# Optimization experiments

Measured on AMD Instinct MI355X. Metric: run time of the kernel, lower is better.

The kernel has to match this reference:

```python
import jax, jax.numpy as jnp
import numpy as np

B, N = 16, 16384
K = 16        # num_keypoints
LATENT = 128
CAGE = 8
BN_EPS = 1e-5


def setup_inputs():
    key = jax.random.key(0)
    ks = jax.random.split(key, 40)
    def rn(i, shape, s=1.0):
        return jax.random.normal(ks[i], shape, dtype=jnp.float32) * s
    inp = {
        "source_points": rn(0, (B, N, 3)),
        "target_points": rn(1, (B, N, 3)),
        "enc_w1": rn(2, (64, 3), 0.3), "enc_b1": rn(3, (64,), 0.1),
        "bn1_gamma": 1.0 + rn(4, (64,), 0.1), "bn1_beta": rn(5, (64,), 0.1),
        "bn1_mean": rn(6, (64,), 0.1), "bn1_var": 0.5 + jax.random.uniform(ks[7], (64,), dtype=jnp.float32),
        "enc_w2": rn(8, (128, 64), 0.1), "enc_b2": rn(9, (128,), 0.1),
        "bn2_gamma": 1.0 + rn(10, (128,), 0.1), "bn2_beta": rn(11, (128,), 0.1),
        "bn2_mean": rn(12, (128,), 0.1), "bn2_var": 0.5 + jax.random.uniform(ks[13], (128,), dtype=jnp.float32),
        "enc_w3": rn(14, (LATENT, 128), 0.1), "enc_b3": rn(15, (LATENT,), 0.1),
        "bn3_gamma": 1.0 + rn(16, (LATENT,), 0.1), "bn3_beta": rn(17, (LATENT,), 0.1),
        "bn3_mean": rn(18, (LATENT,), 0.1), "bn3_var": 0.5 + jax.random.uniform(ks[19], (LATENT,), dtype=jnp.float32),
        "kp_w1": rn(20, (128, LATENT), 0.1), "kp_b1": rn(21, (128,), 0.1),
        "kp_w2": rn(22, (K * 3, 128), 0.1), "kp_b2": rn(23, (K * 3,), 0.1),
        "cg_w1": rn(24, (128, K * 3), 0.1), "cg_b1": rn(25, (128,), 0.1),
        "cg_w2": rn(26, (CAGE ** 3 * 3, 128), 0.05), "cg_b2": rn(27, (CAGE ** 3 * 3,), 0.01),
    }
    return inp


def _bn(x, g, b, m, v):
    # inference-mode BatchNorm1d over channel (last) dim
    return (x - m) * jax.lax.rsqrt(v + BN_EPS) * g + b


def _encode(pts, w1, b1, g1, be1, m1, v1, w2, b2, g2, be2, m2, v2, w3, b3, g3, be3, m3, v3):
    # pointwise 1x1 convs == per-point linear layers; pts: (B, N, 3)
    h = jax.nn.relu(_bn(jnp.einsum('bnc,oc->bno', pts, w1) + b1, g1, be1, m1, v1))
    h = jax.nn.relu(_bn(jnp.einsum('bnc,oc->bno', h, w2) + b2, g2, be2, m2, v2))
    h = jax.nn.relu(_bn(jnp.einsum('bnc,oc->bno', h, w3) + b3, g3, be3, m3, v3))
    return h.max(axis=1)  # global max-pool -> (B, LATENT)


def _fps_one(pts, kps):
    # pts: (N,3), kps: (K,3). Same math as the torch loop: iterative farthest-point
    # selection; recomputing cdist to selected[:i] each step == incremental min-dist.
    # squared distances preserve argmax/min of euclidean distances.
    d0 = jnp.sum((pts[:, None, :] - kps[None, :, :]) ** 2, -1).min(axis=1)
    sel0 = pts[jnp.argmax(d0)]
    mind = jnp.sum((pts - sel0) ** 2, -1)
    def step(mind, _):
        sel = pts[jnp.argmax(mind)]
        return jnp.minimum(mind, jnp.sum((pts - sel) ** 2, -1)), sel
    _, sels = jax.lax.scan(step, mind, None, length=K - 1)
    return jnp.concatenate([sel0[None], sels], axis=0)  # (K, 3)


def _fps(points, keypoints):
    return jax.vmap(_fps_one)(points, keypoints)


def _cage_deform(pts, disp):
    # pts: (B,N,3), disp: (B,C,C,C,3). Batched trilinear interpolation on the cage.
    C = CAGE
    lin = jnp.linspace(0.0, 1.0, C)
    grid = jnp.stack(jnp.meshgrid(lin, lin, lin, indexing='ij'), axis=-1)
    cage = grid[None] + disp
    cf = cage.reshape(cage.shape[0], C * C * C, 3)
    pmin = pts.min(axis=1, keepdims=True)
    pmax = pts.max(axis=1, keepdims=True)
    t = (pts - pmin) / (pmax - pmin + 1e-6) * (C - 1)
    idx = jnp.clip(t.astype(jnp.int32), 0, C - 2)   # trunc == floor (t >= 0)
    w = t - idx.astype(t.dtype)
    u, v, z = idx[..., 0], idx[..., 1], idx[..., 2]
    wx, wy, wz = w[..., 0:1], w[..., 1:2], w[..., 2:3]
    def corner(du, dv, dz):
        flat = (u + du) * C * C + (v + dv) * C + (z + dz)      # (B,N)
        flat = jnp.broadcast_to(flat[..., None], flat.shape + (3,))
        return jnp.take_along_axis(cf, flat, axis=1)            # (B,N,3)
    d = ((1 - wx) * (1 - wy) * (1 - wz) * corner(0, 0, 0)
         + wx * (1 - wy) * (1 - wz) * corner(1, 0, 0)
         + (1 - wx) * wy * (1 - wz) * corner(0, 1, 0)
         + wx * wy * (1 - wz) * corner(1, 1, 0)
         + (1 - wx) * (1 - wy) * wz * corner(0, 0, 1)
         + wx * (1 - wy) * wz * corner(1, 0, 1)
         + (1 - wx) * wy * wz * corner(0, 1, 1)
         + wx * wy * wz * corner(1, 1, 1))
    return pts + d


def reference(source_points, target_points, enc_w1, enc_b1, bn1_gamma, bn1_beta, bn1_mean, bn1_var, enc_w2, enc_b2, bn2_gamma, bn2_beta, bn2_mean, bn2_var, enc_w3, enc_b3, bn3_gamma, bn3_beta, bn3_mean, bn3_var, kp_w1, kp_b1, kp_w2, kp_b2, cg_w1, cg_b1, cg_w2, cg_b2):
    enc = lambda p: _encode(p, enc_w1, enc_b1, bn1_gamma, bn1_beta, bn1_mean, bn1_var,
                            enc_w2, enc_b2, bn2_gamma, bn2_beta, bn2_mean, bn2_var,
                            enc_w3, enc_b3, bn3_gamma, bn3_beta, bn3_mean, bn3_var)
    src_lat = enc(source_points)
    tgt_lat = enc(target_points)
    kp = lambda lat: (jax.nn.relu(lat @ kp_w1.T + kp_b1) @ kp_w2.T + kp_b2).reshape(-1, K, 3)
    src_kp = _fps(source_points, kp(src_lat))
    tgt_kp = _fps(target_points, kp(tgt_lat))
    diff = (tgt_kp - src_kp).reshape(-1, K * 3)
    disp = (jax.nn.relu(diff @ cg_w1.T + cg_b1) @ cg_w2.T + cg_b2).reshape(-1, CAGE, CAGE, CAGE, 3)
    deformed = _cage_deform(source_points, disp)
    return (deformed, src_kp, tgt_kp)
```

## Files before the change

kernel.cpp:

```cpp
#include <hip/hip_runtime.h>

#define B_ 16
#define N_ 16384
#define K_ 16

enum : int {
  WS_LAT  = 0,
  WS_SEL  = 5632,
  WS_PMIN = 7168,
  WS_PMAX = 7216,
  WS_CF   = 7264,
  WS_W1F  = 31840,
  WS_B1F  = 32032,
  WS_WB2H = 32096,
  WS_WB2L = 36192,
  WS_B2F  = 40288,
  WS_WB3H = 40416,
  WS_B3F  = 56800,
  WS_WB3L = 56928,
  WS_END  = 73312
};

enum : int { OUT_DEF=0, OUT_SRCKP=786432, OUT_TGTKP=787200 };

typedef _Float16 f16x8 __attribute__((ext_vector_type(8)));
typedef _Float16 f16x2 __attribute__((ext_vector_type(2)));
typedef float    f32x4 __attribute__((ext_vector_type(4)));

__device__ __forceinline__ float dist2rn(float px,float py,float pz,float sx,float sy,float sz){
  float dx=__fsub_rn(px,sx), dy=__fsub_rn(py,sy), dz=__fsub_rn(pz,sz);
  return __fadd_rn(__fadd_rn(__fmul_rn(dx,dx),__fmul_rn(dy,dy)),__fmul_rn(dz,dz));
}

__device__ __forceinline__ unsigned enc_ord(float x){
  unsigned u = __float_as_uint(x);
  return (u & 0x80000000u) ? ~u : (u | 0x80000000u);
}
__device__ __forceinline__ float dec_ord(unsigned e){
  return __uint_as_float((e & 0x80000000u) ? (e & 0x7fffffffu) : ~e);
}

struct EncW {
  const float *w1,*b1,*g1,*be1,*m1,*v1;
  const float *w2,*b2,*g2,*be2,*m2,*v2;
  const float *w3,*b3,*g3,*be3,*m3,*v3;
};

__device__ __forceinline__ float bn_scale(const float* g, const float* v, int ch){
  return g[ch] * (1.0f / sqrtf(v[ch] + 1e-5f));
}

__global__ void prep_kernel(EncW a, float* ws){
  const int stride = gridDim.x*blockDim.x;
  const int tid = blockIdx.x*blockDim.x + threadIdx.x;
  for (int i=tid;i<4096;i+=stride)
    ws[WS_LAT+i] = 0.0f;
  for (int i=tid;i<48;i+=stride){
    ((unsigned*)ws)[WS_PMIN+i] = 0xFFFFFFFFu;
    ((unsigned*)ws)[WS_PMAX+i] = 0u;
  }
  for (int i=tid;i<192;i+=stride){
    int o=i/3;
    ws[WS_W1F+i] = a.w1[i] * bn_scale(a.g1,a.v1,o);
  }
  for (int i=tid;i<64;i+=stride){
    float s = bn_scale(a.g1,a.v1,i);
    ws[WS_B1F+i] = (a.b1[i] - a.m1[i])*s + a.be1[i];
  }
  for (int i=tid;i<8192;i+=stride){
    int j = i & 7, frag = i >> 3;
    int l = frag & 63, nk = frag >> 6;
    int kt = nk & 1, nt = nk >> 1;
    int c = kt*32 + ((l>>4)<<3) + j;
    int o = nt*16 + (l&15);
    float v = a.w2[o*64+c] * bn_scale(a.g2,a.v2,o);
    _Float16 h = (_Float16)v;
    ((_Float16*)(ws+WS_WB2H))[i] = h;
    ((_Float16*)(ws+WS_WB2L))[i] = (_Float16)(v - (float)h);
  }
  for (int i=tid;i<128;i+=stride){
    float s = bn_scale(a.g2,a.v2,i);
    ws[WS_B2F+i] = (a.b2[i] - a.m2[i])*s + a.be2[i];
  }
  for (int i=tid;i<32768;i+=stride){
    int j = i & 7, frag = i >> 3;
    int l = frag & 63, nk = frag >> 6;
    int kt = nk & 3, nt = nk >> 2;
    int c = kt*32 + ((l>>4)<<3) + j;
    int o = nt*16 + (l&15);
    float v = a.w3[o*128+c] * bn_scale(a.g3,a.v3,o);
    _Float16 h = (_Float16)v;
    ((_Float16*)(ws+WS_WB3H))[i] = h;
    ((_Float16*)(ws+WS_WB3L))[i] = (_Float16)(v - (float)h);
  }
  for (int i=tid;i<128;i+=stride){
    float s = bn_scale(a.g3,a.v3,i);
    ws[WS_B3F+i] = (a.b3[i] - a.m3[i])*s + a.be3[i];
  }
}

__global__ __launch_bounds__(256) void minmax_kernel(const float* __restrict__ src,
                                                     float* __restrict__ ws){
  const int b = blockIdx.y, c = blockIdx.x, t = threadIdx.x;
  const float4* b4 = (const float4*)(src + (size_t)b*N_*3 + (size_t)c*2048*3 + (size_t)t*24);
  float a[24];
  #pragma unroll
  for (int q=0;q<6;q++){ float4 v=b4[q]; a[q*4]=v.x; a[q*4+1]=v.y; a[q*4+2]=v.z; a[q*4+3]=v.w; }
  float mn[3]={3.4e38f,3.4e38f,3.4e38f}, mx[3]={-3.4e38f,-3.4e38f,-3.4e38f};
  #pragma unroll
  for (int k=0;k<8;k++){
    mn[0]=fminf(mn[0],a[k*3  ]); mx[0]=fmaxf(mx[0],a[k*3  ]);
    mn[1]=fminf(mn[1],a[k*3+1]); mx[1]=fmaxf(mx[1],a[k*3+1]);
    mn[2]=fminf(mn[2],a[k*3+2]); mx[2]=fmaxf(mx[2],a[k*3+2]);
  }
  #pragma unroll
  for (int m=1;m<64;m<<=1){
    #pragma unroll
    for (int cc=0;cc<3;cc++){
      mn[cc]=fminf(mn[cc],__shfl_xor(mn[cc],m,64));
      mx[cc]=fmaxf(mx[cc],__shfl_xor(mx[cc],m,64));
    }
  }
  if ((t&63)==0){
    unsigned* wsu = (unsigned*)ws;
    #pragma unroll
    for (int cc=0;cc<3;cc++){
      atomicMin(&wsu[WS_PMIN + b*3 + cc], enc_ord(mn[cc]));
      atomicMax(&wsu[WS_PMAX + b*3 + cc], enc_ord(mx[cc]));
    }
  }
}

__global__ __launch_bounds__(256, 4) void encode_kernel(const float* __restrict__ src,
                                                        const float* __restrict__ tgt,
                                                        const float* __restrict__ ws,
                                                        float* __restrict__ lat){
  const int cloud = blockIdx.y;
  const int tile  = blockIdx.x;
  const int t = threadIdx.x;
  const int lane = t & 63;
  const int wn = __builtin_amdgcn_readfirstlane(t >> 6);
  const int lr = lane & 15;
  const int lg = lane >> 4;

  __shared__ alignas(16) _Float16 A[16384];
  _Float16* AH1 = A;
  _Float16* AL1 = A + 4096;
  _Float16* AH2 = A;
  _Float16* AL2 = A + 8192;

  const float* base = ((cloud < B_) ? (src + (size_t)cloud*N_*3)
                                    : (tgt + (size_t)(cloud-B_)*N_*3))
                      + (size_t)tile*64*3;

  {
    const int pt = t >> 2, q = t & 3;
    const float x = base[pt*3+0], y = base[pt*3+1], z = base[pt*3+2];
    const float* w1 = ws + WS_W1F;
    const float* b1 = ws + WS_B1F;
    const int swz = (pt & 7) << 3;
    #pragma unroll
    for (int cc = 0; cc < 16; cc += 2){
      const int o = q*16 + cc;
      float v0 = fmaf(w1[o*3+2], z, fmaf(w1[o*3+1], y, w1[o*3+0]*x)) + b1[o];
      float v1 = fmaf(w1[o*3+5], z, fmaf(w1[o*3+4], y, w1[o*3+3]*x)) + b1[o+1];
      v0 = fmaxf(v0, 0.0f); v1 = fmaxf(v1, 0.0f);
      f16x2 h, l;
      h[0] = (_Float16)v0;              h[1] = (_Float16)v1;
      l[0] = (_Float16)(v0 - (float)h[0]); l[1] = (_Float16)(v1 - (float)h[1]);
      const int idx = (pt*64 + o) ^ swz;
      *(f16x2*)&AH1[idx] = h;
      *(f16x2*)&AL1[idx] = l;
    }
  }
  __syncthreads();

  f32x4 acc2[4][2];
  #pragma unroll
  for (int m=0;m<4;m++){
    #pragma unroll
    for (int n=0;n<2;n++) acc2[m][n] = (f32x4){0.f,0.f,0.f,0.f};
  }
  {
    const _Float16* wb2h = (const _Float16*)(ws + WS_WB2H);
    const _Float16* wb2l = (const _Float16*)(ws + WS_WB2L);
    const int swz = (lr & 7) << 3;
    #pragma unroll
    for (int kt=0; kt<2; kt++){
      f16x8 bh[2], bl[2];
      #pragma unroll
      for (int n=0;n<2;n++){
        const int fi = (((wn*2+n)*2 + kt)*64 + lane)*8;
        bh[n] = *(const f16x8*)(wb2h + fi);
        bl[n] = *(const f16x8*)(wb2l + fi);
      }
      #pragma unroll
      for (int m=0;m<4;m++){
        const int row = m*16 + lr;
        const int idx = (row*64 + kt*32 + lg*8) ^ swz;
        const f16x8 ah = *(const f16x8*)&AH1[idx];
        const f16x8 al = *(const f16x8*)&AL1[idx];
        #pragma unroll
        for (int n=0;n<2;n++){
          acc2[m][n] = __builtin_amdgcn_mfma_f32_16x16x32_f16(ah, bh[n], acc2[m][n], 0,0,0);
          acc2[m][n] = __builtin_amdgcn_mfma_f32_16x16x32_f16(ah, bl[n], acc2[m][n], 0,0,0);
          acc2[m][n] = __builtin_amdgcn_mfma_f32_16x16x32_f16(al, bh[n], acc2[m][n], 0,0,0);
        }
      }
    }
  }
  __syncthreads();

  {
    const float* b2 = ws + WS_B2F;
    #pragma unroll
    for (int n=0;n<2;n++){
      const int ch = wn*32 + n*16 + lr;
      const float b = b2[ch];
      #pragma unroll
      for (int m=0;m<4;m++){
        #pragma unroll
        for (int r=0;r<4;r++){
          const int row = m*16 + lg*4 + r;
          const float v = fmaxf(acc2[m][n][r] + b, 0.0f);
          const _Float16 hi = (_Float16)v;
          const _Float16 lo = (_Float16)(v - (float)hi);
          const int idx = (row*128 + ch) ^ ((row & 7) << 3);
          AH2[idx] = hi;
          AL2[idx] = lo;
        }
      }
    }
  }
  __syncthreads();

  f32x4 acc3[4][2];
  #pragma unroll
  for (int m=0;m<4;m++){
    #pragma unroll
    for (int n=0;n<2;n++) acc3[m][n] = (f32x4){0.f,0.f,0.f,0.f};
  }
  {
    const _Float16* wb3h = (const _Float16*)(ws + WS_WB3H);
    const _Float16* wb3l = (const _Float16*)(ws + WS_WB3L);
    const int swz = (lr & 7) << 3;
    #pragma unroll
    for (int kt=0; kt<4; kt++){
      f16x8 bh[2], bl[2];
      #pragma unroll
      for (int n=0;n<2;n++){
        const int fi = (((wn*2+n)*4 + kt)*64 + lane)*8;
        bh[n] = *(const f16x8*)(wb3h + fi);
        bl[n] = *(const f16x8*)(wb3l + fi);
      }
      #pragma unroll
      for (int m=0;m<4;m++){
        const int row = m*16 + lr;
        const int idx = (row*128 + kt*32 + lg*8) ^ swz;
        const f16x8 ah = *(const f16x8*)&AH2[idx];
        const f16x8 al = *(const f16x8*)&AL2[idx];
        #pragma unroll
        for (int n=0;n<2;n++){
          acc3[m][n] = __builtin_amdgcn_mfma_f32_16x16x32_f16(ah, bh[n], acc3[m][n], 0,0,0);
          acc3[m][n] = __builtin_amdgcn_mfma_f32_16x16x32_f16(ah, bl[n], acc3[m][n], 0,0,0);
          acc3[m][n] = __builtin_amdgcn_mfma_f32_16x16x32_f16(al, bh[n], acc3[m][n], 0,0,0);
        }
      }
    }
  }

  {
    const float* b3 = ws + WS_B3F;
    #pragma unroll
    for (int n=0;n<2;n++){
      const int ch = wn*32 + n*16 + lr;
      const float b = b3[ch];
      float x = 0.0f;
      #pragma unroll
      for (int m=0;m<4;m++){
        #pragma unroll
        for (int r=0;r<4;r++)
          x = fmaxf(x, acc3[m][n][r] + b);
      }
      x = fmaxf(x, __shfl_xor(x, 16, 64));
      x = fmaxf(x, __shfl_xor(x, 32, 64));
      if (lane < 16)
        atomicMax((unsigned*)(lat + cloud*128 + ch), __float_as_uint(x));
    }
  }
}

__device__ __forceinline__ void fps_round(int r, int t, int wv,
                                          float bv, int bi, float bx, float by, float bz,
                                          float (*cv)[16], int (*ci)[16],
                                          float (*cx)[16], float (*cy)[16], float (*cz)[16],
                                          float* ws, float* out, int cloud,
                                          float& s0, float& s1, float& s2){
  float v = bv; int i = bi;
  #pragma unroll
  for (int m=1;m<64;m<<=1){
    float v2=__shfl_xor(v,m,64); int i2=__shfl_xor(i,m,64);
    if (v2 > v || (v2 == v && i2 < i)){ v=v2; i=i2; }
  }
  const int p = r & 1;
  if ((i >> 4) == t){ cv[p][wv]=v; ci[p][wv]=i; cx[p][wv]=bx; cy[p][wv]=by; cz[p][wv]=bz; }
  __syncthreads();
  float wvv = cv[p][0]; int wi = ci[p][0]; int ws_slot = 0;
  #pragma unroll
  for (int e=1;e<16;e++){
    float v2=cv[p][e]; int i2=ci[p][e];
    if (v2 > wvv || (v2 == wvv && i2 < wi)){ wvv=v2; wi=i2; ws_slot=e; }
  }
  s0 = cx[p][ws_slot]; s1 = cy[p][ws_slot]; s2 = cz[p][ws_slot];
  if (t == 0){
    float* sw = ws + WS_SEL + cloud*48 + r*3;
    sw[0]=s0; sw[1]=s1; sw[2]=s2;
    size_t o = (cloud<B_) ? (size_t)(OUT_SRCKP + cloud*48 + r*3)
                          : (size_t)(OUT_TGTKP + (cloud-B_)*48 + r*3);
    out[o]=s0; out[o+1]=s1; out[o+2]=s2;
  }
}

__global__ __launch_bounds__(1024) void fps_kernel(const float* __restrict__ src,
                                                   const float* __restrict__ tgt,
                                                   const float* __restrict__ kw1,
                                                   const float* __restrict__ kb1,
                                                   const float* __restrict__ kw2,
                                                   const float* __restrict__ kb2,
                                                   float* ws, float* out){
  const int cloud = blockIdx.x; const int t = threadIdx.x;
  const int wv = t >> 6;
  const float* base = (cloud < B_) ? (src + (size_t)cloud*N_*3)
                                   : (tgt + (size_t)(cloud-B_)*N_*3);
  __shared__ float kpl[48];
  __shared__ float h[128];
  __shared__ float cv[2][16]; __shared__ int ci[2][16];
  __shared__ float cx[2][16]; __shared__ float cy[2][16]; __shared__ float cz[2][16];

  float px[16], py[16], pz[16];
  {
    const float4* b4 = (const float4*)(base + (size_t)t*48);
    float a[48];
    #pragma unroll
    for (int q=0;q<12;q++){ float4 v=b4[q]; a[q*4]=v.x; a[q*4+1]=v.y; a[q*4+2]=v.z; a[q*4+3]=v.w; }
    #pragma unroll
    for (int k=0;k<16;k++){ px[k]=a[k*3]; py[k]=a[k*3+1]; pz[k]=a[k*3+2]; }
  }

  const float* lat = ws + WS_LAT + cloud*128;
  if (t < 128){
    float acc = kb1[t];
    const float* w = kw1 + t*128;
    for (int c=0;c<128;c++) acc = fmaf(lat[c], w[c], acc);
    h[t] = fmaxf(acc, 0.0f);
  }
  __syncthreads();
  if (t < 48){
    float acc = kb2[t];
    const float* w = kw2 + t*128;
    for (int c=0;c<128;c++) acc = fmaf(h[c], w[c], acc);
    kpl[t] = acc;
  }
  __syncthreads();

  float mind[16];
  #pragma unroll
  for (int k=0;k<16;k++) mind[k] = 3.4028235e38f;
  for (int j=0;j<K_;j++){
    const float sx=kpl[j*3], sy=kpl[j*3+1], sz=kpl[j*3+2];
    #pragma unroll
    for (int k=0;k<16;k++)
      mind[k] = fminf(mind[k], dist2rn(px[k],py[k],pz[k], sx,sy,sz));
  }

  float bv = -1.0f; int bi = 0; float bx=0.f, by=0.f, bz=0.f;
  #pragma unroll
  for (int k=0;k<16;k++){
    if (mind[k] > bv){ bv=mind[k]; bi=t*16+k; bx=px[k]; by=py[k]; bz=pz[k]; }
  }
  float s0, s1, s2;
  fps_round(0, t, wv, bv, bi, bx, by, bz, cv, ci, cx, cy, cz, ws, out, cloud, s0, s1, s2);

  bv = -1.0f; bi = 0;
  #pragma unroll
  for (int k=0;k<16;k++){
    float d = dist2rn(px[k],py[k],pz[k], s0,s1,s2);
    mind[k] = d;
    if (d > bv){ bv=d; bi=t*16+k; bx=px[k]; by=py[k]; bz=pz[k]; }
  }
  fps_round(1, t, wv, bv, bi, bx, by, bz, cv, ci, cx, cy, cz, ws, out, cloud, s0, s1, s2);

  for (int r=2; r<K_; ++r){
    bv = -1.0f; bi = 0;
    #pragma unroll
    for (int k=0;k<16;k++){
      float d = dist2rn(px[k],py[k],pz[k], s0,s1,s2);
      float m = fminf(mind[k], d);
      mind[k] = m;
      if (m > bv){ bv=m; bi=t*16+k; bx=px[k]; by=py[k]; bz=pz[k]; }
    }
    fps_round(r, t, wv, bv, bi, bx, by, bz, cv, ci, cx, cy, cz, ws, out, cloud, s0, s1, s2);
  }
}

__global__ void cage_mlp_kernel(const float* __restrict__ ws,
                                const float* __restrict__ cw1, const float* __restrict__ cb1,
                                const float* __restrict__ cw2, const float* __restrict__ cb2,
                                float* __restrict__ wsm){
  const int b = blockIdx.x >> 2, part = blockIdx.x & 3;
  const int t = threadIdx.x;
  __shared__ float diff[48]; __shared__ float h[128];
  if (t<48) diff[t] = __fsub_rn(ws[WS_SEL + (B_+b)*48 + t], ws[WS_SEL + b*48 + t]);
  __syncthreads();
  if (t<128){
    const float* w = cw1 + t*48;
    float acc = cb1[t];
    for (int j=0;j<48;j++) acc = fmaf(diff[j], w[j], acc);
    h[t] = fmaxf(acc, 0.0f);
  }
  __syncthreads();
  for (int o = part*384 + t; o < part*384 + 384; o += 256){
    const float* w = cw2 + o*128;
    float acc = cb2[o];
    for (int c=0;c<128;c++) acc = fmaf(h[c], w[c], acc);
    int flat = o/3, coord = o - flat*3;
    int u = flat>>6, v=(flat>>3)&7, z=flat&7;
    int g = (coord==0)?u:((coord==1)?v:z);
    float gv = (g==7)?1.0f:(float)g*(1.0f/7.0f);
    wsm[WS_CF + b*1536 + o] = gv + acc;
  }
}

__global__ __launch_bounds__(256) void deform_kernel(const float* __restrict__ src,
                                                     const float* __restrict__ ws,
                                                     float* __restrict__ out){
  const int b = blockIdx.y;
  const int n = blockIdx.x*256 + threadIdx.x;
  __shared__ float cf[1536];
  for (int i=threadIdx.x;i<1536;i+=256) cf[i] = ws[WS_CF + b*1536 + i];
  __syncthreads();

  const float* p = src + ((size_t)b*N_ + n)*3;
  float pt[3]; int id[3]; float w[3];
  #pragma unroll
  for (int c=0;c<3;c++){
    float pv = p[c];
    float mn  = dec_ord(((const unsigned*)ws)[WS_PMIN+b*3+c]);
    float mxv = dec_ord(((const unsigned*)ws)[WS_PMAX+b*3+c]);
    float denom = __fadd_rn(__fsub_rn(mxv, mn), 1e-6f);
    float tc = __fmul_rn(__fdiv_rn(__fsub_rn(pv, mn), denom), 7.0f);
    int ic = (int)tc; ic = min(max(ic,0),6);
    pt[c]=pv; id[c]=ic; w[c]=__fsub_rn(tc, (float)ic);
  }
  const int flat = (id[0]<<6) + (id[1]<<3) + id[2];
  const float* c000 = cf + flat*3;
  const float wx=w[0], wy=w[1], wz=w[2];
  const float ux=__fsub_rn(1.0f,wx), uy=__fsub_rn(1.0f,wy), uz=__fsub_rn(1.0f,wz);
  const float w000=__fmul_rn(__fmul_rn(ux,uy),uz);
  const float w100=__fmul_rn(__fmul_rn(wx,uy),uz);
  const float w010=__fmul_rn(__fmul_rn(ux,wy),uz);
  const float w110=__fmul_rn(__fmul_rn(wx,wy),uz);
  const float w001=__fmul_rn(__fmul_rn(ux,uy),wz);
  const float w101=__fmul_rn(__fmul_rn(wx,uy),wz);
  const float w011=__fmul_rn(__fmul_rn(ux,wy),wz);
  const float w111=__fmul_rn(__fmul_rn(wx,wy),wz);
  #pragma unroll
  for (int c=0;c<3;c++){
    float d = __fmul_rn(w000, c000[c]);
    d = __fadd_rn(d, __fmul_rn(w100, c000[192+c]));
    d = __fadd_rn(d, __fmul_rn(w010, c000[24+c]));
    d = __fadd_rn(d, __fmul_rn(w110, c000[216+c]));
    d = __fadd_rn(d, __fmul_rn(w001, c000[3+c]));
    d = __fadd_rn(d, __fmul_rn(w101, c000[195+c]));
    d = __fadd_rn(d, __fmul_rn(w011, c000[27+c]));
    d = __fadd_rn(d, __fmul_rn(w111, c000[219+c]));
    out[((size_t)b*N_+n)*3 + c] = __fadd_rn(pt[c], d);
  }
}

extern "C" void kernel_launch(void* const* d_in, const int* in_sizes, int n_in,
                              void* d_out, int out_size, void* d_ws, size_t ws_size,
                              hipStream_t stream){
  const float* src = (const float*)d_in[0];
  const float* tgt = (const float*)d_in[1];
  float* ws = (float*)d_ws;
  float* out = (float*)d_out;

  EncW ew;
  ew.w1 =(const float*)d_in[2];  ew.b1 =(const float*)d_in[3];
  ew.g1 =(const float*)d_in[4];  ew.be1=(const float*)d_in[5];
  ew.m1 =(const float*)d_in[6];  ew.v1 =(const float*)d_in[7];
  ew.w2 =(const float*)d_in[8];  ew.b2 =(const float*)d_in[9];
  ew.g2 =(const float*)d_in[10]; ew.be2=(const float*)d_in[11];
  ew.m2 =(const float*)d_in[12]; ew.v2 =(const float*)d_in[13];
  ew.w3 =(const float*)d_in[14]; ew.b3 =(const float*)d_in[15];
  ew.g3 =(const float*)d_in[16]; ew.be3=(const float*)d_in[17];
  ew.m3 =(const float*)d_in[18]; ew.v3 =(const float*)d_in[19];

  prep_kernel<<<128, 256, 0, stream>>>(ew, ws);
  minmax_kernel<<<dim3(8,16), 256, 0, stream>>>(src, ws);
  encode_kernel<<<dim3(256,32), 256, 0, stream>>>(src, tgt, ws, ws + WS_LAT);
  fps_kernel<<<32, 1024, 0, stream>>>(src, tgt,
      (const float*)d_in[20], (const float*)d_in[21],
      (const float*)d_in[22], (const float*)d_in[23], ws, out);
  cage_mlp_kernel<<<64, 256, 0, stream>>>(ws,
      (const float*)d_in[24], (const float*)d_in[25],
      (const float*)d_in[26], (const float*)d_in[27], ws);
  deform_kernel<<<dim3(64,16), 256, 0, stream>>>(src, ws, out);
}
```

Before: 319.3 us.

## Fuse minmax, FPS, cage MLP and deform into one per-batch tail kernel

Measured after the change: 449.0 us. 40.6% more time.

```diff
diff --git a/kernel.cpp b/kernel.cpp
--- a/kernel.cpp
+++ b/kernel.cpp
@@ -6,10 +6,6 @@
 
 enum : int {
   WS_LAT  = 0,
-  WS_SEL  = 5632,
-  WS_PMIN = 7168,
-  WS_PMAX = 7216,
-  WS_CF   = 7264,
   WS_W1F  = 31840,
   WS_B1F  = 32032,
   WS_WB2H = 32096,
@@ -32,14 +28,6 @@
   return __fadd_rn(__fadd_rn(__fmul_rn(dx,dx),__fmul_rn(dy,dy)),__fmul_rn(dz,dz));
 }
 
-__device__ __forceinline__ unsigned enc_ord(float x){
-  unsigned u = __float_as_uint(x);
-  return (u & 0x80000000u) ? ~u : (u | 0x80000000u);
-}
-__device__ __forceinline__ float dec_ord(unsigned e){
-  return __uint_as_float((e & 0x80000000u) ? (e & 0x7fffffffu) : ~e);
-}
-
 struct EncW {
   const float *w1,*b1,*g1,*be1,*m1,*v1;
   const float *w2,*b2,*g2,*be2,*m2,*v2;
@@ -55,10 +43,6 @@
   const int tid = blockIdx.x*blockDim.x + threadIdx.x;
   for (int i=tid;i<4096;i+=stride)
     ws[WS_LAT+i] = 0.0f;
-  for (int i=tid;i<48;i+=stride){
-    ((unsigned*)ws)[WS_PMIN+i] = 0xFFFFFFFFu;
-    ((unsigned*)ws)[WS_PMAX+i] = 0u;
-  }
   for (int i=tid;i<192;i+=stride){
     int o=i/3;
     ws[WS_W1F+i] = a.w1[i] * bn_scale(a.g1,a.v1,o);
@@ -96,38 +80,6 @@
   for (int i=tid;i<128;i+=stride){
     float s = bn_scale(a.g3,a.v3,i);
     ws[WS_B3F+i] = (a.b3[i] - a.m3[i])*s + a.be3[i];
-  }
-}
-
-__global__ __launch_bounds__(256) void minmax_kernel(const float* __restrict__ src,
-                                                     float* __restrict__ ws){
-  const int b = blockIdx.y, c = blockIdx.x, t = threadIdx.x;
-  const float4* b4 = (const float4*)(src + (size_t)b*N_*3 + (size_t)c*2048*3 + (size_t)t*24);
-  float a[24];
-  #pragma unroll
-  for (int q=0;q<6;q++){ float4 v=b4[q]; a[q*4]=v.x; a[q*4+1]=v.y; a[q*4+2]=v.z; a[q*4+3]=v.w; }
-  float mn[3]={3.4e38f,3.4e38f,3.4e38f}, mx[3]={-3.4e38f,-3.4e38f,-3.4e38f};
-  #pragma unroll
-  for (int k=0;k<8;k++){
-    mn[0]=fminf(mn[0],a[k*3  ]); mx[0]=fmaxf(mx[0],a[k*3  ]);
-    mn[1]=fminf(mn[1],a[k*3+1]); mx[1]=fmaxf(mx[1],a[k*3+1]);
-    mn[2]=fminf(mn[2],a[k*3+2]); mx[2]=fmaxf(mx[2],a[k*3+2]);
-  }
-  #pragma unroll
-  for (int m=1;m<64;m<<=1){
-    #pragma unroll
-    for (int cc=0;cc<3;cc++){
-      mn[cc]=fminf(mn[cc],__shfl_xor(mn[cc],m,64));
-      mx[cc]=fmaxf(mx[cc],__shfl_xor(mx[cc],m,64));
-    }
-  }
-  if ((t&63)==0){
-    unsigned* wsu = (unsigned*)ws;
-    #pragma unroll
-    for (int cc=0;cc<3;cc++){
-      atomicMin(&wsu[WS_PMIN + b*3 + cc], enc_ord(mn[cc]));
-      atomicMax(&wsu[WS_PMAX + b*3 + cc], enc_ord(mx[cc]));
-    }
   }
 }
 
@@ -290,12 +242,12 @@
   }
 }
 
-__device__ __forceinline__ void fps_round(int r, int t, int wv,
-                                          float bv, int bi, float bx, float by, float bz,
-                                          float (*cv)[16], int (*ci)[16],
-                                          float (*cx)[16], float (*cy)[16], float (*cz)[16],
-                                          float* ws, float* out, int cloud,
-                                          float& s0, float& s1, float& s2){
+__device__ __forceinline__ void fps_round_t(int r, int t, int wv,
+                                            float bv, int bi, float bx, float by, float bz,
+                                            float (*cv)[16], int (*ci)[16],
+                                            float (*cx)[16], float (*cy)[16], float (*cz)[16],
+                                            float* sel_buf, float* out, size_t out_base,
+                                            float& s0, float& s1, float& s2){
   float v = bv; int i = bi;
   #pragma unroll
   for (int m=1;m<64;m<<=1){
@@ -305,112 +257,153 @@
   const int p = r & 1;
   if ((i >> 4) == t){ cv[p][wv]=v; ci[p][wv]=i; cx[p][wv]=bx; cy[p][wv]=by; cz[p][wv]=bz; }
   __syncthreads();
-  float wvv = cv[p][0]; int wi = ci[p][0]; int ws_slot = 0;
+  float wvv = cv[p][0]; int wi = ci[p][0]; int slot = 0;
   #pragma unroll
   for (int e=1;e<16;e++){
     float v2=cv[p][e]; int i2=ci[p][e];
-    if (v2 > wvv || (v2 == wvv && i2 < wi)){ wvv=v2; wi=i2; ws_slot=e; }
-  }
-  s0 = cx[p][ws_slot]; s1 = cy[p][ws_slot]; s2 = cz[p][ws_slot];
+    if (v2 > wvv || (v2 == wvv && i2 < wi)){ wvv=v2; wi=i2; slot=e; }
+  }
+  s0 = cx[p][slot]; s1 = cy[p][slot]; s2 = cz[p][slot];
   if (t == 0){
-    float* sw = ws + WS_SEL + cloud*48 + r*3;
-    sw[0]=s0; sw[1]=s1; sw[2]=s2;
-    size_t o = (cloud<B_) ? (size_t)(OUT_SRCKP + cloud*48 + r*3)
-                          : (size_t)(OUT_TGTKP + (cloud-B_)*48 + r*3);
-    out[o]=s0; out[o+1]=s1; out[o+2]=s2;
-  }
-}
-
-__global__ __launch_bounds__(1024) void fps_kernel(const float* __restrict__ src,
-                                                   const float* __restrict__ tgt,
-                                                   const float* __restrict__ kw1,
-                                                   const float* __restrict__ kb1,
-                                                   const float* __restrict__ kw2,
-                                                   const float* __restrict__ kb2,
-                                                   float* ws, float* out){
-  const int cloud = blockIdx.x; const int t = threadIdx.x;
+    sel_buf[r*3]=s0; sel_buf[r*3+1]=s1; sel_buf[r*3+2]=s2;
+    out[out_base + r*3]=s0; out[out_base + r*3+1]=s1; out[out_base + r*3+2]=s2;
+  }
+}
+
+__global__ __launch_bounds__(1024) void tail_kernel(const float* __restrict__ src,
+                                                    const float* __restrict__ tgt,
+                                                    const float* __restrict__ kw1,
+                                                    const float* __restrict__ kb1,
+                                                    const float* __restrict__ kw2,
+                                                    const float* __restrict__ kb2,
+                                                    const float* __restrict__ cw1,
+                                                    const float* __restrict__ cb1,
+                                                    const float* __restrict__ cw2,
+                                                    const float* __restrict__ cb2,
+                                                    const float* __restrict__ ws,
+                                                    float* __restrict__ out){
+  const int b = blockIdx.x;
+  const int t = threadIdx.x;
   const int wv = t >> 6;
-  const float* base = (cloud < B_) ? (src + (size_t)cloud*N_*3)
-                                   : (tgt + (size_t)(cloud-B_)*N_*3);
+  const int lane = t & 63;
+
   __shared__ float kpl[48];
   __shared__ float h[128];
   __shared__ float cv[2][16]; __shared__ int ci[2][16];
   __shared__ float cx[2][16]; __shared__ float cy[2][16]; __shared__ float cz[2][16];
-
-  float px[16], py[16], pz[16];
-  {
-    const float4* b4 = (const float4*)(base + (size_t)t*48);
-    float a[48];
-    #pragma unroll
-    for (int q=0;q<12;q++){ float4 v=b4[q]; a[q*4]=v.x; a[q*4+1]=v.y; a[q*4+2]=v.z; a[q*4+3]=v.w; }
-    #pragma unroll
-    for (int k=0;k<16;k++){ px[k]=a[k*3]; py[k]=a[k*3+1]; pz[k]=a[k*3+2]; }
-  }
-
-  const float* lat = ws + WS_LAT + cloud*128;
-  if (t < 128){
-    float acc = kb1[t];
-    const float* w = kw1 + t*128;
-    for (int c=0;c<128;c++) acc = fmaf(lat[c], w[c], acc);
-    h[t] = fmaxf(acc, 0.0f);
-  }
-  __syncthreads();
-  if (t < 48){
-    float acc = kb2[t];
-    const float* w = kw2 + t*128;
-    for (int c=0;c<128;c++) acc = fmaf(h[c], w[c], acc);
-    kpl[t] = acc;
-  }
-  __syncthreads();
-
-  float mind[16];
-  #pragma unroll
-  for (int k=0;k<16;k++) mind[k] = 3.4028235e38f;
-  for (int j=0;j<K_;j++){
-    const float sx=kpl[j*3], sy=kpl[j*3+1], sz=kpl[j*3+2];
-    #pragma unroll
-    for (int k=0;k<16;k++)
-      mind[k] = fminf(mind[k], dist2rn(px[k],py[k],pz[k], sx,sy,sz));
-  }
-
-  float bv = -1.0f; int bi = 0; float bx=0.f, by=0.f, bz=0.f;
-  #pragma unroll
-  for (int k=0;k<16;k++){
-    if (mind[k] > bv){ bv=mind[k]; bi=t*16+k; bx=px[k]; by=py[k]; bz=pz[k]; }
-  }
-  float s0, s1, s2;
-  fps_round(0, t, wv, bv, bi, bx, by, bz, cv, ci, cx, cy, cz, ws, out, cloud, s0, s1, s2);
-
-  bv = -1.0f; bi = 0;
-  #pragma unroll
-  for (int k=0;k<16;k++){
-    float d = dist2rn(px[k],py[k],pz[k], s0,s1,s2);
-    mind[k] = d;
-    if (d > bv){ bv=d; bi=t*16+k; bx=px[k]; by=py[k]; bz=pz[k]; }
-  }
-  fps_round(1, t, wv, bv, bi, bx, by, bz, cv, ci, cx, cy, cz, ws, out, cloud, s0, s1, s2);
-
-  for (int r=2; r<K_; ++r){
+  __shared__ float sel_src[48]; __shared__ float sel_tgt[48];
+  __shared__ float red[96];
+  __shared__ float pmn[3]; __shared__ float pmx[3];
+  __shared__ float cf[1536];
+
+  for (int half=0; half<2; ++half){
+    const int cloud = b + half*B_;
+    const float* base = (half==0) ? (src + (size_t)b*N_*3) : (tgt + (size_t)b*N_*3);
+
+    float px[16], py[16], pz[16];
+    float mn0=3.4e38f,mn1=3.4e38f,mn2=3.4e38f, mx0=-3.4e38f,mx1=-3.4e38f,mx2=-3.4e38f;
+    {
+      const float4* b4 = (const float4*)(base + (size_t)t*48);
+      #pragma unroll
+      for (int q=0;q<4;q++){
+        float4 va=b4[q*3], vb=b4[q*3+1], vc=b4[q*3+2];
+        px[q*4  ]=va.x; py[q*4  ]=va.y; pz[q*4  ]=va.z;
+        px[q*4+1]=va.w; py[q*4+1]=vb.x; pz[q*4+1]=vb.y;
+        px[q*4+2]=vb.z; py[q*4+2]=vb.w; pz[q*4+2]=vc.x;
+        px[q*4+3]=vc.y; py[q*4+3]=vc.z; pz[q*4+3]=vc.w;
+      }
+    }
+
+    if (half==0){
+      #pragma unroll
+      for (int k=0;k<16;k++){
+        mn0=fminf(mn0,px[k]); mn1=fminf(mn1,py[k]); mn2=fminf(mn2,pz[k]);
+        mx0=fmaxf(mx0,px[k]); mx1=fmaxf(mx1,py[k]); mx2=fmaxf(mx2,pz[k]);
+      }
+      #pragma unroll
+      for (int m=1;m<64;m<<=1){
+        mn0=fminf(mn0,__shfl_xor(mn0,m,64)); mx0=fmaxf(mx0,__shfl_xor(mx0,m,64));
+        mn1=fminf(mn1,__shfl_xor(mn1,m,64)); mx1=fmaxf(mx1,__shfl_xor(mx1,m,64));
+        mn2=fminf(mn2,__shfl_xor(mn2,m,64)); mx2=fmaxf(mx2,__shfl_xor(mx2,m,64));
+      }
+      if (lane==0){
+        red[wv*6+0]=mn0; red[wv*6+1]=mn1; red[wv*6+2]=mn2;
+        red[wv*6+3]=mx0; red[wv*6+4]=mx1; red[wv*6+5]=mx2;
+      }
+      __syncthreads();
+      if (t==0){
+        float a0=red[0],a1=red[1],a2=red[2],a3=red[3],a4=red[4],a5=red[5];
+        for (int e=1;e<16;e++){
+          a0=fminf(a0,red[e*6+0]); a1=fminf(a1,red[e*6+1]); a2=fminf(a2,red[e*6+2]);
+          a3=fmaxf(a3,red[e*6+3]); a4=fmaxf(a4,red[e*6+4]); a5=fmaxf(a5,red[e*6+5]);
+        }
+        pmn[0]=a0; pmn[1]=a1; pmn[2]=a2; pmx[0]=a3; pmx[1]=a4; pmx[2]=a5;
+      }
+    }
+
+    const float* lat = ws + WS_LAT + cloud*128;
+    __syncthreads();
+    if (t < 128){
+      float acc = kb1[t];
+      const float* w = kw1 + t*128;
+      for (int c=0;c<128;c++) acc = fmaf(lat[c], w[c], acc);
+      h[t] = fmaxf(acc, 0.0f);
+    }
+    __syncthreads();
+    if (t < 48){
+      float acc = kb2[t];
+      const float* w = kw2 + t*128;
+      for (int c=0;c<128;c++) acc = fmaf(h[c], w[c], acc);
+      kpl[t] = acc;
+    }
+    __syncthreads();
+
+    float mind[16];
+    #pragma unroll
+    for (int k=0;k<16;k++) mind[k] = 3.4028235e38f;
+    for (int j=0;j<K_;j++){
+      const float sx=kpl[j*3], sy=kpl[j*3+1], sz=kpl[j*3+2];
+      #pragma unroll
+      for (int k=0;k<16;k++)
+        mind[k] = fminf(mind[k], dist2rn(px[k],py[k],pz[k], sx,sy,sz));
+    }
+
+    float* sel_buf = (half==0) ? sel_src : sel_tgt;
+    const size_t out_base = (half==0) ? (size_t)(OUT_SRCKP + b*48) : (size_t)(OUT_TGTKP + b*48);
+
+    float bv = -1.0f; int bi = 0; float bx=0.f, by=0.f, bz=0.f;
+    #pragma unroll
+    for (int k=0;k<16;k++){
+      if (mind[k] > bv){ bv=mind[k]; bi=t*16+k; bx=px[k]; by=py[k]; bz=pz[k]; }
+    }
+    float s0, s1, s2;
+    fps_round_t(0, t, wv, bv, bi, bx, by, bz, cv, ci, cx, cy, cz, sel_buf, out, out_base, s0, s1, s2);
+
     bv = -1.0f; bi = 0;
     #pragma unroll
     for (int k=0;k<16;k++){
       float d = dist2rn(px[k],py[k],pz[k], s0,s1,s2);
-      float m = fminf(mind[k], d);
-      mind[k] = m;
-      if (m > bv){ bv=m; bi=t*16+k; bx=px[k]; by=py[k]; bz=pz[k]; }
-    }
-    fps_round(r, t, wv, bv, bi, bx, by, bz, cv, ci, cx, cy, cz, ws, out, cloud, s0, s1, s2);
-  }
-}
-
-__global__ void cage_mlp_kernel(const float* __restrict__ ws,
-                                const float* __restrict__ cw1, const float* __restrict__ cb1,
-                                const float* __restrict__ cw2, const float* __restrict__ cb2,
-                                float* __restrict__ wsm){
-  const int b = blockIdx.x >> 2, part = blockIdx.x & 3;
-  const int t = threadIdx.x;
-  __shared__ float diff[48]; __shared__ float h[128];
-  if (t<48) diff[t] = __fsub_rn(ws[WS_SEL + (B_+b)*48 + t], ws[WS_SEL + b*48 + t]);
+      mind[k] = d;
+      if (d > bv){ bv=d; bi=t*16+k; bx=px[k]; by=py[k]; bz=pz[k]; }
+    }
+    fps_round_t(1, t, wv, bv, bi, bx, by, bz, cv, ci, cx, cy, cz, sel_buf, out, out_base, s0, s1, s2);
+
+    for (int r=2; r<K_; ++r){
+      bv = -1.0f; bi = 0;
+      #pragma unroll
+      for (int k=0;k<16;k++){
+        float d = dist2rn(px[k],py[k],pz[k], s0,s1,s2);
+        float m = fminf(mind[k], d);
+        mind[k] = m;
+        if (m > bv){ bv=m; bi=t*16+k; bx=px[k]; by=py[k]; bz=pz[k]; }
+      }
+      fps_round_t(r, t, wv, bv, bi, bx, by, bz, cv, ci, cx, cy, cz, sel_buf, out, out_base, s0, s1, s2);
+    }
+    __syncthreads();
+  }
+
+  __shared__ float diff[48];
+  if (t<48) diff[t] = __fsub_rn(sel_tgt[t], sel_src[t]);
   __syncthreads();
   if (t<128){
     const float* w = cw1 + t*48;
@@ -419,7 +412,7 @@
     h[t] = fmaxf(acc, 0.0f);
   }
   __syncthreads();
-  for (int o = part*384 + t; o < part*384 + 384; o += 256){
+  for (int o = t; o < 1536; o += 1024){
     const float* w = cw2 + o*128;
     float acc = cb2[o];
     for (int c=0;c<128;c++) acc = fmaf(h[c], w[c], acc);
@@ -427,54 +420,52 @@
     int u = flat>>6, v=(flat>>3)&7, z=flat&7;
     int g = (coord==0)?u:((coord==1)?v:z);
     float gv = (g==7)?1.0f:(float)g*(1.0f/7.0f);
-    wsm[WS_CF + b*1536 + o] = gv + acc;
-  }
-}
-
-__global__ __launch_bounds__(256) void deform_kernel(const float* __restrict__ src,
-                                                     const float* __restrict__ ws,
-                                                     float* __restrict__ out){
-  const int b = blockIdx.y;
-  const int n = blockIdx.x*256 + threadIdx.x;
-  __shared__ float cf[1536];
-  for (int i=threadIdx.x;i<1536;i+=256) cf[i] = ws[WS_CF + b*1536 + i];
-  __syncthreads();
-
-  const float* p = src + ((size_t)b*N_ + n)*3;
-  float pt[3]; int id[3]; float w[3];
-  #pragma unroll
-  for (int c=0;c<3;c++){
-    float pv = p[c];
-    float mn  = dec_ord(((const unsigned*)ws)[WS_PMIN+b*3+c]);
-    float mxv = dec_ord(((const unsigned*)ws)[WS_PMAX+b*3+c]);
-    float denom = __fadd_rn(__fsub_rn(mxv, mn), 1e-6f);
-    float tc = __fmul_rn(__fdiv_rn(__fsub_rn(pv, mn), denom), 7.0f);
-    int ic = (int)tc; ic = min(max(ic,0),6);
-    pt[c]=pv; id[c]=ic; w[c]=__fsub_rn(tc, (float)ic);
-  }
-  const int flat = (id[0]<<6) + (id[1]<<3) + id[2];
-  const float* c000 = cf + flat*3;
-  const float wx=w[0], wy=w[1], wz=w[2];
-  const float ux=__fsub_rn(1.0f,wx), uy=__fsub_rn(1.0f,wy), uz=__fsub_rn(1.0f,wz);
-  const float w000=__fmul_rn(__fmul_rn(ux,uy),uz);
-  const float w100=__fmul_rn(__fmul_rn(wx,uy),uz);
-  const float w010=__fmul_rn(__fmul_rn(ux,wy),uz);
-  const float w110=__fmul_rn(__fmul_rn(wx,wy),uz);
-  const float w001=__fmul_rn(__fmul_rn(ux,uy),wz);
-  const float w101=__fmul_rn(__fmul_rn(wx,uy),wz);
-  const float w011=__fmul_rn(__fmul_rn(ux,wy),wz);
-  const float w111=__fmul_rn(__fmul_rn(wx,wy),wz);
-  #pragma unroll
-  for (int c=0;c<3;c++){
-    float d = __fmul_rn(w000, c000[c]);
-    d = __fadd_rn(d, __fmul_rn(w100, c000[192+c]));
-    d = __fadd_rn(d, __fmul_rn(w010, c000[24+c]));
-    d = __fadd_rn(d, __fmul_rn(w110, c000[216+c]));
-    d = __fadd_rn(d, __fmul_rn(w001, c000[3+c]));
-    d = __fadd_rn(d, __fmul_rn(w101, c000[195+c]));
-    d = __fadd_rn(d, __fmul_rn(w011, c000[27+c]));
-    d = __fadd_rn(d, __fmul_rn(w111, c000[219+c]));
-    out[((size_t)b*N_+n)*3 + c] = __fadd_rn(pt[c], d);
+    cf[o] = gv + acc;
+  }
+  __syncthreads();
+
+  const float q0n=pmn[0], q1n=pmn[1], q2n=pmn[2];
+  const float q0x=pmx[0], q1x=pmx[1], q2x=pmx[2];
+  const float* sbase = src + (size_t)b*N_*3;
+  float* obase = out + OUT_DEF + (size_t)b*N_*3;
+  for (int k=0;k<16;k++){
+    const int n = t + k*1024;
+    const float* p = sbase + (size_t)n*3;
+    float pt[3]; int id[3]; float w[3];
+    #pragma unroll
+    for (int c=0;c<3;c++){
+      float pv = p[c];
+      float mnv = (c==0)?q0n:((c==1)?q1n:q2n);
+      float mxv = (c==0)?q0x:((c==1)?q1x:q2x);
+      float denom = __fadd_rn(__fsub_rn(mxv, mnv), 1e-6f);
+      float tc = __fmul_rn(__fdiv_rn(__fsub_rn(pv, mnv), denom), 7.0f);
+      int ic = (int)tc; ic = min(max(ic,0),6);
+      pt[c]=pv; id[c]=ic; w[c]=__fsub_rn(tc, (float)ic);
+    }
+    const int flat = (id[0]<<6) + (id[1]<<3) + id[2];
+    const float* c000 = cf + flat*3;
+    const float wx=w[0], wy=w[1], wz=w[2];
+    const float ux=__fsub_rn(1.0f,wx), uy=__fsub_rn(1.0f,wy), uz=__fsub_rn(1.0f,wz);
+    const float w000=__fmul_rn(__fmul_rn(ux,uy),uz);
+    const float w100=__fmul_rn(__fmul_rn(wx,uy),uz);
+    const float w010=__fmul_rn(__fmul_rn(ux,wy),uz);
+    const float w110=__fmul_rn(__fmul_rn(wx,wy),uz);
+    const float w001=__fmul_rn(__fmul_rn(ux,uy),wz);
+    const float w101=__fmul_rn(__fmul_rn(wx,uy),wz);
+    const float w011=__fmul_rn(__fmul_rn(ux,wy),wz);
+    const float w111=__fmul_rn(__fmul_rn(wx,wy),wz);
+    #pragma unroll
+    for (int c=0;c<3;c++){
+      float d = __fmul_rn(w000, c000[c]);
+      d = __fadd_rn(d, __fmul_rn(w100, c000[192+c]));
+      d = __fadd_rn(d, __fmul_rn(w010, c000[24+c]));
+      d = __fadd_rn(d, __fmul_rn(w110, c000[216+c]));
+      d = __fadd_rn(d, __fmul_rn(w001, c000[3+c]));
+      d = __fadd_rn(d, __fmul_rn(w101, c000[195+c]));
+      d = __fadd_rn(d, __fmul_rn(w011, c000[27+c]));
+      d = __fadd_rn(d, __fmul_rn(w111, c000[219+c]));
+      obase[(size_t)n*3 + c] = __fadd_rn(pt[c], d);
+    }
   }
 }
 
@@ -498,13 +489,10 @@
   ew.m3 =(const float*)d_in[18]; ew.v3 =(const float*)d_in[19];
 
   prep_kernel<<<128, 256, 0, stream>>>(ew, ws);
-  minmax_kernel<<<dim3(8,16), 256, 0, stream>>>(src, ws);
   encode_kernel<<<dim3(256,32), 256, 0, stream>>>(src, tgt, ws, ws + WS_LAT);
-  fps_kernel<<<32, 1024, 0, stream>>>(src, tgt,
+  tail_kernel<<<16, 1024, 0, stream>>>(src, tgt,
       (const float*)d_in[20], (const float*)d_in[21],
-      (const float*)d_in[22], (const float*)d_in[23], ws, out);
-  cage_mlp_kernel<<<64, 256, 0, stream>>>(ws,
+      (const float*)d_in[22], (const float*)d_in[23],
       (const float*)d_in[24], (const float*)d_in[25],
-      (const float*)d_in[26], (const float*)d_in[27], ws);
-  deform_kernel<<<dim3(64,16), 256, 0, stream>>>(src, ws, out);
-}
+      (const float*)d_in[26], (const float*)d_in[27], ws, out);
+}
```
